# Kernel optimization log

Measured on AMD Instinct MI355X. Metric: run time of the kernel, lower is better.

The kernel has to match this reference:

```python
import jax, jax.numpy as jnp
import numpy as np
from jax import lax

ALPHA = 0.5
KERNEL = 25
NUM_P = 16
SEQ_LEN = 1440
PRED_LEN = 720
DWT_LEN = SEQ_LEN // 2 + 2            # 722 (pytorch_wavelets zero-mode, sym3 filt len 6)
FREQ = int(np.ceil(DWT_LEN / 2 * ALPHA) * 2)  # 362

_DEC_LO = np.array([0.035226291882100656, -0.08544127388224149, -0.13501102001039084,
                    0.4598775021193313, 0.8068915093133388, 0.3326705529509569], np.float32)
_DEC_HI = np.array([-0.3326705529509569, 0.8068915093133388, -0.4598775021193313,
                    -0.13501102001039084, 0.08544127388224149, 0.035226291882100656], np.float32)
DEC_LO, DEC_HI = jnp.asarray(_DEC_LO), jnp.asarray(_DEC_HI)
REC_LO, REC_HI = DEC_LO[::-1], DEC_HI[::-1]


def dwt1(x):
    # pytorch_wavelets DWT1DForward(J=1, mode='zero'): zero-pad then stride-2 true conv with dec filters
    B, C, L = x.shape
    out = (L + 5) // 2
    p = 2 * (out - 1) - L + 6
    xp = jnp.pad(x.reshape(B * C, 1, L), ((0, 0), (0, 0), (p // 2, p - p // 2)))
    ker = jnp.stack([DEC_LO[::-1], DEC_HI[::-1]])[:, None, :]   # (2,1,6); xcorr w/ reversed == conv
    y = lax.conv_general_dilated(xp, ker, (2,), 'VALID', dimension_numbers=('NCH', 'OIH', 'NCH'))
    return y[:, 0].reshape(B, C, out), y[:, 1].reshape(B, C, out)


def iwt1(lo, hi):
    # DWT1DInverse mode='zero': conv_transpose stride 2, padding L-2  ->  dilate + conv, pad 1
    B, C, n = lo.shape
    z = jnp.concatenate([lo.reshape(B * C, 1, n), hi.reshape(B * C, 1, n)], axis=1)
    ker = jnp.stack([REC_LO[::-1], REC_HI[::-1]])[None, :, :]   # (O=1, I=2, 6)
    y = lax.conv_general_dilated(z, ker, (1,), [(1, 1)], lhs_dilation=(2,),
                                 dimension_numbers=('NCH', 'OIH', 'NCH'))
    return y[:, 0].reshape(B, C, 2 * n - 4)


def mov_avg(x, k=KERNEL):
    pooled = lax.reduce_window(x, 0.0, lax.add, (1, 1, k), (1, 1, 1), 'VALID') / k
    return jnp.pad(pooled, ((0, 0), (0, 0), (k // 2, k // 2 - (k + 1) % 2)), mode='edge')


def mov_norm(x):
    mean = lax.stop_gradient(mov_avg(x))
    xc = lax.stop_gradient(x - mean)
    std = lax.stop_gradient(mov_avg(jnp.abs(xc))) + 1e-5
    return xc / std, mean, std


def inst_norm(x):
    mean = lax.stop_gradient(jnp.mean(x, -1, keepdims=True))
    xc = x - mean
    var = jnp.mean((xc - jnp.mean(xc, -1, keepdims=True)) ** 2, -1, keepdims=True)
    return xc / jnp.sqrt(var + 1e-5)


def mean_std_mlp(mean, std, mp, sp, mw1, mw2, sw1, sw2, mpred, spred):
    m_all = jnp.mean(mean, -1, keepdims=True)
    s_all = jnp.mean(std, -1, keepdims=True)
    mr = (mean - m_all) @ mp.T
    sr = (std - s_all) @ sp.T
    mr = jax.nn.relu(mr @ mw1.T) @ mw2.T
    sr = jax.nn.relu(sr @ sw1.T) @ sw2.T
    mean_o = mr @ mpred.T + m_all
    std_o = jax.nn.relu(sr @ spred.T + s_all) + 1e-5
    return mean_o, std_o


def forward(x, latent_w, latent_b, acp, dcp):
    xt = jnp.swapaxes(x, -1, 1)                    # (B, C, L)
    ac0, dc0 = dwt1(xt)                            # (B, C, DWT_LEN)
    ac_n = inst_norm(ac0)
    ac, m_ac, s_ac = mov_norm(ac0)
    dc, m_dc, s_dc = mov_norm(dc0)
    m_ac, s_ac = mean_std_mlp(m_ac, s_ac, *acp)    # MLPs[-1]
    m_dc, s_dc = mean_std_mlp(m_dc, s_dc, *dcp)    # MLPs[0]
    dcF = jnp.fft.fft(dc)
    acF = jnp.fft.fft(ac_n)
    idx = jnp.argsort(-jnp.abs(acF), axis=-1)[..., :FREQ]
    amp = ALPHA * jnp.take_along_axis(acF, idx, -1) + (1.0 - ALPHA) * jnp.take_along_axis(dcF, idx, -1)
    B, C, _ = dcF.shape
    bi = jnp.arange(B)[:, None, None]
    ci = jnp.arange(C)[None, :, None]
    dcF = dcF.at[bi, ci, idx].set(amp)
    dc = jnp.real(jnp.fft.ifft(dcF))
    xr = iwt1(ac, dc)                              # (B, C, SEQ_LEN)
    mean = iwt1(m_ac, m_dc)                        # (B, C, PRED_LEN)
    std = iwt1(s_ac, s_dc)
    xr = xr.reshape(B, C, NUM_P, SEQ_LEN // NUM_P)
    emb = xr @ latent_w.T + latent_b               # (B, C, NUM_P, d_model)
    return emb, mean, std


def setup_inputs() -> dict:
    key = jax.random.key(0)
    B, C = 64, 128
    d_model, d_ff = 512, 1024
    s = 0.02
    names_shapes = [
        ('x', (B, SEQ_LEN, C), 1.0),
        ('latent_w', (d_model, SEQ_LEN // NUM_P), s),
    ]
    for pre in ('ac', 'dc'):
        names_shapes += [
            (pre + '_mean_proj', (d_model, DWT_LEN), s),
            (pre + '_std_proj', (d_model, DWT_LEN), s),
            (pre + '_mean_ffn_w1', (d_ff, d_model), s),
            (pre + '_mean_ffn_w2', (d_model, d_ff), s),
            (pre + '_std_ffn_w1', (d_ff, d_model), s),
            (pre + '_std_ffn_w2', (d_model, d_ff), s),
            (pre + '_mean_pred', (PRED_LEN // 2 + 2, d_model), s),
            (pre + '_std_pred', (PRED_LEN // 2 + 2, d_model), s),
        ]
    keys = jax.random.split(key, len(names_shapes))
    inp = {n: jax.random.normal(k, shp, dtype=jnp.float32) * sc
           for (n, shp, sc), k in zip(names_shapes, keys)}
    inp['latent_b'] = jnp.zeros((d_model,), jnp.float32)
    return inp


def reference(x, latent_w, latent_b,
              ac_mean_proj, ac_std_proj, ac_mean_ffn_w1, ac_mean_ffn_w2,
              ac_std_ffn_w1, ac_std_ffn_w2, ac_mean_pred, ac_std_pred,
              dc_mean_proj, dc_std_proj, dc_mean_ffn_w1, dc_mean_ffn_w2,
              dc_std_ffn_w1, dc_std_ffn_w2, dc_mean_pred, dc_std_pred):
    acp = (ac_mean_proj, ac_std_proj, ac_mean_ffn_w1, ac_mean_ffn_w2,
           ac_std_ffn_w1, ac_std_ffn_w2, ac_mean_pred, ac_std_pred)
    dcp = (dc_mean_proj, dc_std_proj, dc_mean_ffn_w1, dc_mean_ffn_w2,
           dc_std_ffn_w1, dc_std_ffn_w2, dc_mean_pred, dc_std_pred)
    return forward(x, latent_w, latent_b, acp, dcp)
```

## Files before the change

### kernel.cpp

```cpp
#include <hip/hip_runtime.h>
#include <cmath>

#define RTOT 8192
#define NDWT 722
#define KP1  736
#define LSEQ 1440
#define NHEAD 362
#define NFREQ 362

typedef __bf16 bf16x8 __attribute__((ext_vector_type(8)));
typedef float f32x4 __attribute__((ext_vector_type(4)));
typedef float f32x2 __attribute__((ext_vector_type(2)));

__device__ __forceinline__ unsigned short f2bf(float f) {
    unsigned u = __float_as_uint(f);
    u += 0x7fffu + ((u >> 16) & 1u);
    return (unsigned short)(u >> 16);
}
__device__ __forceinline__ float bf2f(unsigned short u) {
    return __uint_as_float(((unsigned)u) << 16);
}

__device__ __forceinline__ void cmac(f32x2& s, f32x2 a, f32x2 w) {
    asm("v_pk_fma_f32 %0, %1, %2, %0 op_sel:[0,0,0] op_sel_hi:[0,1,1]\n\t"
        "v_pk_fma_f32 %0, %1, %2, %0 op_sel:[1,1,0] op_sel_hi:[1,0,1] neg_lo:[0,1,0]"
        : "+v"(s) : "v"(a), "v"(w));
}
__device__ __forceinline__ void cmac2(f32x2& s, f32x2 u, f32x2 v, f32x2 w) {
    asm("v_pk_fma_f32 %0, %1, %3, %0 op_sel:[0,0,0] op_sel_hi:[1,0,1]\n\t"
        "v_pk_fma_f32 %0, %2, %3, %0 op_sel:[1,1,0] op_sel_hi:[0,1,1] neg_lo:[0,1,0]"
        : "+v"(s) : "v"(u), "v"(v), "v"(w));
}
__device__ __forceinline__ f32x2 cmul(f32x2 a, f32x2 b) {
    f32x2 r;
    asm("v_pk_mul_f32 %0, %1, %2 op_sel:[0,0] op_sel_hi:[0,1]\n\t"
        "v_pk_fma_f32 %0, %1, %2, %0 op_sel:[1,1,0] op_sel_hi:[1,0,1] neg_lo:[0,1,0]"
        : "=&v"(r) : "v"(a), "v"(b));
    return r;
}

__constant__ float c_lo[6] = {0.035226291882100656f, -0.08544127388224149f, -0.13501102001039084f,
                              0.4598775021193313f, 0.8068915093133388f, 0.3326705529509569f};
__constant__ float c_hi[6] = {-0.3326705529509569f, 0.8068915093133388f, -0.4598775021193313f,
                              -0.13501102001039084f, 0.08544127388224149f, 0.035226291882100656f};

struct CvtDesc { const float* src; unsigned short* dst; int N, K, Np, Kp; };
struct CvtArgs { CvtDesc d[17]; float2* wtab; };
__global__ __launch_bounds__(256) void cvt_all_kernel(CvtArgs a) {
    if (blockIdx.y == 17) {
        int m = blockIdx.x * 256 + threadIdx.x;
        if (m < NDWT) {
            double ang = -2.0 * 3.141592653589793238462643383279502884 * (double)m / (double)NDWT;
            a.wtab[m] = make_float2((float)cos(ang), (float)sin(ang));
        }
        return;
    }
    CvtDesc d = a.d[blockIdx.y];
    int idx = blockIdx.x * 256 + threadIdx.x;
    int tot = d.Np * d.Kp;
    if (idx >= tot) return;
    int r = idx / d.Kp, c = idx - r * d.Kp;
    float v = (r < d.N && c < d.K) ? d.src[(size_t)r * d.K + c] : 0.f;
    d.dst[idx] = f2bf(v);
}

__global__ __launch_bounds__(256) void dwt_kernel(const float* __restrict__ x,
                                                  float* __restrict__ ac0,
                                                  float* __restrict__ dc0) {
    __shared__ float xs[68][129];
    const int b = blockIdx.x;
    const int t0 = blockIdx.y * 32;
    const int tid = threadIdx.x;
    const int lbase = 2 * t0 - 4;
    for (int i = tid; i < 68 * 32; i += 256) {
        int ri = i >> 5;
        int c4 = (i & 31) * 4;
        int l = lbase + ri;
        float4 v = make_float4(0.f, 0.f, 0.f, 0.f);
        if (l >= 0 && l < LSEQ)
            v = *reinterpret_cast<const float4*>(&x[((size_t)b * LSEQ + l) * 128 + c4]);
        xs[ri][c4] = v.x; xs[ri][c4 + 1] = v.y; xs[ri][c4 + 2] = v.z; xs[ri][c4 + 3] = v.w;
    }
    __syncthreads();
    const int tt = tid & 31;
    const int t = t0 + tt;
    const int cw = tid >> 5;
    if (t < NDWT) {
        #pragma unroll 4
        for (int co = 0; co < 16; co++) {
            int c = co * 8 + cw;
            float slo = 0.f, shi = 0.f;
            #pragma unroll
            for (int j = 0; j < 6; j++) {
                float v = xs[2 * tt + 5 - j][c];
                slo += v * c_lo[j];
                shi += v * c_hi[j];
            }
            size_t o = ((size_t)b * 128 + c) * NDWT + t;
            ac0[o] = slo;
            dc0[o] = shi;
        }
    }
}

__device__ __forceinline__ float blockSum256(float v, float* red) {
    #pragma unroll
    for (int o = 32; o > 0; o >>= 1) v += __shfl_down(v, o, 64);
    int lane = threadIdx.x & 63, wid = threadIdx.x >> 6;
    __syncthreads();
    if (lane == 0) red[wid] = v;
    __syncthreads();
    return red[0] + red[1] + red[2] + red[3];
}

template <bool ABS>
__device__ __forceinline__ void pool25(const float* rowv, float* pool, int tid) {
    int i0 = tid * 3;
    if (i0 < 698) {
        float s25 = 0.f;
        #pragma unroll
        for (int j = 0; j < 25; j++) { float v = rowv[i0 + j]; s25 += ABS ? fabsf(v) : v; }
        pool[i0] = s25 * (1.f / 25.f);
        #pragma unroll
        for (int qq = 1; qq < 3; qq++) {
            int i = i0 + qq;
            if (i < 698) {
                float vin = rowv[i + 24], vout = rowv[i - 1];
                s25 += (ABS ? fabsf(vin) : vin) - (ABS ? fabsf(vout) : vout);
                pool[i] = s25 * (1.f / 25.f);
            }
        }
    }
}

__device__ void fft722_dev(f32x2* X, f32x2* T, const f32x2* Wt, const f32x2* W19) {
    const int tid = threadIdx.x;
    if (tid < 190) {
        const int c = tid / 38;
        const int g = tid - c * 38;
        const int p = (g >= 19) ? 1 : 0;
        const int rr = g - 19 * p;
        const int t0 = c * 4;
        const int nt = (c == 4) ? 3 : 4;
        const f32x2* xp = X + 2 * rr + p;
        f32x2 st[4], w[4], s[4];
        f32x2 a0 = xp[0];
        #pragma unroll
        for (int i = 0; i < 4; i++) {
            int ti = t0 + i; if (ti > 18) ti = 0;
            st[i] = W19[ti];
            w[i] = st[i];
            s[i] = a0;
        }
        #pragma unroll
        for (int m = 1; m <= 9; m++) {
            f32x2 a = xp[38 * m];
            f32x2 b = xp[38 * (19 - m)];
            f32x2 u = a + b, v = a - b;
            #pragma unroll
            for (int i = 0; i < 4; i++) {
                cmac2(s[i], u, v, w[i]);
                if (m < 9) w[i] = cmul(w[i], st[i]);
            }
        }
        int m0 = rr * t0;
        f32x2* Tp = T + p * 361 + rr * 19 + t0;
        #pragma unroll
        for (int i = 0; i < 4; i++) {
            if (i < nt) Tp[i] = cmul(s[i], Wt[2 * m0]);
            m0 += rr;
        }
    }
    __syncthreads();
    if (tid < 190) {
        const int c = tid / 38;
        const int g = tid - c * 38;
        const int p = (g >= 19) ? 1 : 0;
        const int t = g - 19 * p;
        const int jj0 = c * 4;
        const int nj = (c == 4) ? 3 : 4;
        const f32x2* Ap = T + p * 361 + t;
        f32x2 st[4], w[4], s[4];
        f32x2 a0 = Ap[0];
        #pragma unroll
        for (int i = 0; i < 4; i++) {
            int jj = jj0 + i; if (jj > 18) jj = 0;
            st[i] = W19[jj];
            w[i] = st[i];
            s[i] = a0;
        }
        #pragma unroll
        for (int m = 1; m <= 9; m++) {
            f32x2 a = Ap[19 * m];
            f32x2 b = Ap[19 * (19 - m)];
            f32x2 u = a + b, v = a - b;
            #pragma unroll
            for (int i = 0; i < 4; i++) {
                cmac2(s[i], u, v, w[i]);
                if (m < 9) w[i] = cmul(w[i], st[i]);
            }
        }
        f32x2* Xp = X + p * 361;
        #pragma unroll
        for (int i = 0; i < 4; i++) {
            int jj = jj0 + i;
            if (i < nj) Xp[t + 19 * jj] = s[i];
        }
    }
    __syncthreads();
    for (int k = tid; k < 361; k += 256) {
        f32x2 e = X[k], o = X[361 + k], w = Wt[k];
        f32x2 tt = {0.f, 0.f};
        cmac(tt, o, w);
        X[k] = e + tt;
        X[361 + k] = e - tt;
    }
    __syncthreads();
}

__global__ __launch_bounds__(256) void stats_fft_kernel(
    const float* __restrict__ ac0in,
    const float* __restrict__ dc0in,
    unsigned short* __restrict__ cent,
    float* __restrict__ stat,
    unsigned short* __restrict__ xrbf,
    const f32x2* __restrict__ Wtab) {
    __shared__ f32x2 Wt[NDWT];
    __shared__ f32x2 W19s[19];
    __shared__ f32x2 B1[NDWT];
    __shared__ float acpL[NDWT];
    __shared__ __align__(16) char arena[8704];
    __shared__ unsigned hist[256];
    __shared__ unsigned suf[256];
    __shared__ unsigned sh_digit, sh_rem;
    f32x2* B2   = (f32x2*)arena;
    float* smag = (float*)(arena + 5776);
    float* row  = (float*)arena;
    float* xc   = (float*)(arena + 2888);
    float* pool = (float*)(arena + 5776);
    float* red  = (float*)(arena + 8568);
    const int r = blockIdx.x, tid = threadIdx.x;
    const int lane = tid & 63;
    const size_t base = (size_t)r * NDWT;
    const size_t baseP = (size_t)r * KP1;
    const size_t CS = (size_t)RTOT * KP1;

    for (int i = tid; i < NDWT; i += 256) Wt[i] = Wtab[i];
    if (tid < 19) W19s[tid] = Wtab[38 * tid];

    for (int i = tid; i < NDWT; i += 256) row[i] = ac0in[base + i];
    __syncthreads();
    float s = 0.f;
    for (int i = tid; i < NDWT; i += 256) s += row[i];
    float mean = blockSum256(s, red) * (1.f / 722.f);
    s = 0.f;
    for (int i = tid; i < NDWT; i += 256) s += row[i] - mean;
    float m2 = blockSum256(s, red) * (1.f / 722.f);
    s = 0.f;
    for (int i = tid; i < NDWT; i += 256) { float d = row[i] - mean - m2; s += d * d; }
    float var = blockSum256(s, red) * (1.f / 722.f);
    float inv = 1.f / sqrtf(var + 1e-5f);
    for (int i = tid; i < NDWT; i += 256) B1[i].x = (row[i] - mean) * inv;

    pool25<false>(row, pool, tid);
    __syncthreads();
    float msum = 0.f;
    for (int l = tid; l < NDWT; l += 256) {
        int pi = l - 12; pi = pi < 0 ? 0 : (pi > 697 ? 697 : pi);
        float m = pool[pi];
        msum += m;
        xc[l] = row[l] - m;
    }
    float m_all = blockSum256(msum, red) * (1.f / 722.f);
    __syncthreads();
    pool25<true>(xc, pool, tid);
    __syncthreads();
    float ssum = 0.f;
    for (int l = tid; l < NDWT; l += 256) {
        int pi = l - 12; pi = pi < 0 ? 0 : (pi > 697 ? 697 : pi);
        float sd = pool[pi] + 1e-5f;
        ssum += sd;
        acpL[l] = xc[l] / sd;
    }
    float s_all = blockSum256(ssum, red) * (1.f / 722.f);
    if (tid == 0) { stat[r] = m_all; stat[RTOT + r] = s_all; }
    for (int l = tid; l < KP1; l += 256) {
        if (l < NDWT) {
            float m = row[l] - xc[l];
            int pi = l - 12; pi = pi < 0 ? 0 : (pi > 697 ? 697 : pi);
            float sd = pool[pi] + 1e-5f;
            cent[baseP + l]      = f2bf(m - m_all);
            cent[CS + baseP + l] = f2bf(sd - s_all);
        } else { cent[baseP + l] = 0; cent[CS + baseP + l] = 0; }
    }
    __syncthreads();

    for (int i = tid; i < NDWT; i += 256) row[i] = dc0in[base + i];
    __syncthreads();
    pool25<false>(row, pool, tid);
    __syncthreads();
    float msum2 = 0.f;
    for (int l = tid; l < NDWT; l += 256) {
        int pi = l - 12; pi = pi < 0 ? 0 : (pi > 697 ? 697 : pi);
        float m = pool[pi];
        msum2 += m;
        xc[l] = row[l] - m;
    }
    float m_all2 = blockSum256(msum2, red) * (1.f / 722.f);
    __syncthreads();
    pool25<true>(xc, pool, tid);
    __syncthreads();
    float ssum2 = 0.f;
    for (int l = tid; l < NDWT; l += 256) {
        int pi = l - 12; pi = pi < 0 ? 0 : (pi > 697 ? 697 : pi);
        float sd = pool[pi] + 1e-5f;
        ssum2 += sd;
        B1[l].y = xc[l] / sd;
    }
    float s_all2 = blockSum256(ssum2, red) * (1.f / 722.f);
    if (tid == 0) { stat[2 * RTOT + r] = m_all2; stat[3 * RTOT + r] = s_all2; }
    for (int l = tid; l < KP1; l += 256) {
        if (l < NDWT) {
            float m = row[l] - xc[l];
            int pi = l - 12; pi = pi < 0 ? 0 : (pi > 697 ? 697 : pi);
            float sd = pool[pi] + 1e-5f;
            cent[2 * CS + baseP + l] = f2bf(m - m_all2);
            cent[3 * CS + baseP + l] = f2bf(sd - s_all2);
        } else { cent[2 * CS + baseP + l] = 0; cent[3 * CS + baseP + l] = 0; }
    }
    __syncthreads();

    fft722_dev(B1, B2, Wt, W19s);
    for (int k = tid; k < 362; k += 256) {
        int m = (NDWT - k) % NDWT;
        f32x2 zk = B1[k], zm = B1[m];
        f32x2 ak = {0.5f * (zk.x + zm.x), 0.5f * (zk.y - zm.y)};
        f32x2 dk = {0.5f * (zk.y + zm.y), 0.5f * (zm.x - zk.x)};
        B1[k] = ak; B2[k] = dk;
        smag[k] = ak.x * ak.x + ak.y * ak.y;
        if (m != k) {
            f32x2 am = {0.5f * (zm.x + zk.x), 0.5f * (zm.y - zk.y)};
            f32x2 dm = {0.5f * (zm.y + zk.y), 0.5f * (zk.x - zm.x)};
            B1[m] = am; B2[m] = dm;
            smag[m] = am.x * am.x + am.y * am.y;
        }
    }
    __syncthreads();

    unsigned prefix = 0, rem = NFREQ;
    for (int shift = 24; shift >= 0; shift -= 8) {
        hist[tid] = 0;
        __syncthreads();
        unsigned hm = (shift == 24) ? 0u : (0xFFFFFFFFu << (shift + 8));
        for (int i = tid; i < NDWT; i += 256) {
            unsigned b = __float_as_uint(smag[i]);
            if ((b & hm) == prefix) atomicAdd(&hist[(b >> shift) & 255], 1u);
        }
        __syncthreads();
        if (tid < 64) {
            unsigned h0 = hist[tid * 4 + 0], h1 = hist[tid * 4 + 1];
            unsigned h2 = hist[tid * 4 + 2], h3 = hist[tid * 4 + 3];
            unsigned tot = h0 + h1 + h2 + h3;
            unsigned tinc = tot;
            #pragma unroll
            for (int off = 1; off < 64; off <<= 1) {
                unsigned v = __shfl_down(tinc, off, 64);
                tinc += (lane + off < 64) ? v : 0u;
            }
            unsigned tail = tinc - tot;
            unsigned S3 = tail + h3;
            unsigned S2 = S3 + h2;
            unsigned S1 = S2 + h1;
            unsigned S0 = S1 + h0;
            if (S0 >= rem && S1 < rem) { sh_digit = (unsigned)(tid * 4 + 0); sh_rem = rem - S1; }
            if (S1 >= rem && S2 < rem) { sh_digit = (unsigned)(tid * 4 + 1); sh_rem = rem - S2; }
            if (S2 >= rem && S3 < rem) { sh_digit = (unsigned)(tid * 4 + 2); sh_rem = rem - S3; }
            if (S3 >= rem && tail < rem) { sh_digit = (unsigned)(tid * 4 + 3); sh_rem = rem - tail; }
        }
        __syncthreads();
        prefix |= (sh_digit << shift);
        rem = sh_rem;
    }
    int c0 = tid * 3, cnt = 0;
    #pragma unroll
    for (int j = 0; j < 3; j++) {
        int i = c0 + j;
        if (i < NDWT && __float_as_uint(smag[i]) == prefix) cnt++;
    }
    suf[tid] = (unsigned)cnt;
    __syncthreads();
    if (tid < 64) {
        unsigned p0 = suf[tid * 4 + 0], p1 = suf[tid * 4 + 1];
        unsigned p2 = suf[tid * 4 + 2], p3 = suf[tid * 4 + 3];
        unsigned tot = p0 + p1 + p2 + p3;
        unsigned pinc = tot;
        #pragma unroll
        for (int off = 1; off < 64; off <<= 1) {
            unsigned v = __shfl_up(pinc, off, 64);
            pinc += (lane >= off) ? v : 0u;
        }
        unsigned head = pinc - tot;
        suf[tid * 4 + 0] = head;
        suf[tid * 4 + 1] = head + p0;
        suf[tid * 4 + 2] = head + p0 + p1;
        suf[tid * 4 + 3] = head + p0 + p1 + p2;
    }
    __syncthreads();
    int myexc = (int)suf[tid], o = 0;
    #pragma unroll
    for (int j = 0; j < 3; j++) {
        int i = c0 + j;
        if (i < NDWT) {
            unsigned b = __float_as_uint(smag[i]);
            int f = (b > prefix) ? 1 : 0;
            if (b == prefix) { if ((unsigned)(myexc + o) < rem) f = 1; o++; }
            smag[i] = f ? 1.f : 0.f;
        }
    }
    __syncthreads();

    for (int i = tid; i < NDWT; i += 256) {
        f32x2 d = B2[i];
        if (smag[i] != 0.f) { f32x2 a = B1[i]; d.x = 0.5f * (a.x + d.x); d.y = 0.5f * (a.y + d.y); }
        B1[i] = f32x2{d.x, -d.y};
    }
    __syncthreads();
    fft722_dev(B1, B2, Wt, W19s);

    const float inv722 = 1.f / 722.f;
    if (tid < 96) {
        int sub = tid / 6, c = 90 + tid % 6;
        xrbf[((size_t)r * 16 + sub) * 96 + c] = 0;
    }
    for (int t = tid; t < LSEQ; t += 256) {
        float sx = 0.f;
        if (t & 1) {
            int j0 = (t - 1) >> 1;
            #pragma unroll
            for (int i = 0; i < 3; i++)
                sx += acpL[j0 + i] * c_lo[2 * i] + (B1[j0 + i].x * inv722) * c_hi[2 * i];
        } else {
            int j0 = t >> 1;
            #pragma unroll
            for (int i = 0; i < 3; i++)
                sx += acpL[j0 + i] * c_lo[2 * i + 1] + (B1[j0 + i].x * inv722) * c_hi[2 * i + 1];
        }
        xrbf[((size_t)r * 16 + t / 90) * 96 + (t % 90)] = f2bf(sx);
    }
}

__global__ __launch_bounds__(256) void iwt_heads_kernel(const unsigned short* __restrict__ heads,
                                                        float* __restrict__ out_mean,
                                                        float* __restrict__ out_std) {
    const int r = blockIdx.x;
    const int y = blockIdx.y;
    const int z = y / 3;
    const int t = (y % 3) * 256 + threadIdx.x;
    if (t >= 720) return;
    const size_t HR = (size_t)RTOT * NHEAD;
    const unsigned short* lp = heads + (size_t)z * HR + (size_t)r * NHEAD;
    const unsigned short* hp = heads + (size_t)(2 + z) * HR + (size_t)r * NHEAD;
    float* out = (z ? out_std : out_mean) + (size_t)r * 720;
    float s = 0.f;
    if (t & 1) {
        int j0 = (t - 1) >> 1;
        #pragma unroll
        for (int i = 0; i < 3; i++) s += bf2f(lp[j0 + i]) * c_lo[2 * i] + bf2f(hp[j0 + i]) * c_hi[2 * i];
    } else {
        int j0 = t >> 1;
        #pragma unroll
        for (int i = 0; i < 3; i++) s += bf2f(lp[j0 + i]) * c_lo[2 * i + 1] + bf2f(hp[j0 + i]) * c_hi[2 * i + 1];
    }
    out[t] = s;
}

struct ZPtrs { const unsigned short* p[4]; };
template <int EPI>
__global__ __launch_bounds__(256) void mfma_gemm_z(
    const unsigned short* __restrict__ A, int lda, size_t zsA,
    ZPtrs Wz, int ldw,
    void* __restrict__ Cout, int ldc, size_t zsC, int Nc,
    const float* __restrict__ biasBase, const float* __restrict__ cbias,
    int Ksteps) {
    __shared__ unsigned short As[2][128 * 32];
    __shared__ unsigned short Bs[2][128 * 32];
    const int z = blockIdx.z;
    const unsigned short* Az = A + (size_t)z * zsA;
    const unsigned short* W = Wz.p[z];
    const int tid = threadIdx.x;
    const int lane = tid & 63, wid = tid >> 6;
    const int bm = blockIdx.x * 128, bn = blockIdx.y * 128;
    const int wr = (wid >> 1) * 64, wc = (wid & 1) * 64;
    f32x4 acc[4][4] = {};
    const int srow = (lane >> 2);
    const int scol = (lane & 3) * 8;
    const int ch0 = wid * 2, ch1 = wid * 2 + 1;
    const unsigned short* ga0 = Az + (size_t)(bm + ch0 * 16 + srow) * lda + scol;
    const unsigned short* ga1 = Az + (size_t)(bm + ch1 * 16 + srow) * lda + scol;
    const unsigned short* gb0 = W + (size_t)(bn + ch0 * 16 + srow) * ldw + scol;
    const unsigned short* gb1 = W + (size_t)(bn + ch1 * 16 + srow) * ldw + scol;

#define STAGE_GL(buf, ks) do { const int k0_ = (ks) * 32;                                      \
    __builtin_amdgcn_global_load_lds((const __attribute__((address_space(1))) unsigned int*)(ga0 + k0_), \
        (__attribute__((address_space(3))) unsigned int*)(&As[buf][ch0 * 512]), 16, 0, 0);     \
    __builtin_amdgcn_global_load_lds((const __attribute__((address_space(1))) unsigned int*)(gb0 + k0_), \
        (__attribute__((address_space(3))) unsigned int*)(&Bs[buf][ch0 * 512]), 16, 0, 0);     \
    __builtin_amdgcn_global_load_lds((const __attribute__((address_space(1))) unsigned int*)(ga1 + k0_), \
        (__attribute__((address_space(3))) unsigned int*)(&As[buf][ch1 * 512]), 16, 0, 0);     \
    __builtin_amdgcn_global_load_lds((const __attribute__((address_space(1))) unsigned int*)(gb1 + k0_), \
        (__attribute__((address_space(3))) unsigned int*)(&Bs[buf][ch1 * 512]), 16, 0, 0);     \
    } while (0)

    STAGE_GL(0, 0);
    int cur = 0;
    const int kof = (lane >> 4) * 8;
    for (int ks = 0; ks < Ksteps; ks++) {
        if (ks + 1 < Ksteps) {
            STAGE_GL(cur ^ 1, ks + 1);
            asm volatile("s_waitcnt vmcnt(4)" ::: "memory");
        } else {
            asm volatile("s_waitcnt vmcnt(0)" ::: "memory");
        }
        __builtin_amdgcn_s_barrier();
        __builtin_amdgcn_sched_barrier(0);
        bf16x8 af[4], bfr[4];
        #pragma unroll
        for (int m = 0; m < 4; m++)
            af[m] = *reinterpret_cast<const bf16x8*>(&As[cur][(wr + m * 16 + (lane & 15)) * 32 + kof]);
        #pragma unroll
        for (int n = 0; n < 4; n++)
            bfr[n] = *reinterpret_cast<const bf16x8*>(&Bs[cur][(wc + n * 16 + (lane & 15)) * 32 + kof]);
        #pragma unroll
        for (int m = 0; m < 4; m++)
            #pragma unroll
            for (int n = 0; n < 4; n++)
                acc[m][n] = __builtin_amdgcn_mfma_f32_16x16x32_bf16(af[m], bfr[n], acc[m][n], 0, 0, 0);
        __builtin_amdgcn_s_barrier();
        __builtin_amdgcn_sched_barrier(0);
        cur ^= 1;
    }
#undef STAGE_GL

    unsigned short* Cb = (unsigned short*)Cout + (size_t)z * zsC;
    float* Cf = (float*)Cout + (size_t)z * zsC;
    const int crow0 = bm + wr + (lane >> 4) * 4;
    const int ccol0 = bn + wc + (lane & 15);
    #pragma unroll
    for (int m = 0; m < 4; m++) {
        #pragma unroll
        for (int n = 0; n < 4; n++) {
            const int col = ccol0 + n * 16;
            if (col < Nc) {
                #pragma unroll
                for (int q = 0; q < 4; q++) {
                    const int row = crow0 + m * 16 + q;
                    float v = acc[m][n][q];
                    if (EPI == 0) {
                        Cb[(size_t)row * ldc + col] = f2bf(v);
                    } else if (EPI == 1) {
                        Cb[(size_t)row * ldc + col] = f2bf(fmaxf(v, 0.f));
                    } else if (EPI == 4) {
                        Cf[(size_t)row * ldc + col] = v + cbias[col];
                    } else {
                        float ob = biasBase[(size_t)z * RTOT + row];
                        if (z & 1) v = fmaxf(v + ob, 0.f) + 1e-5f;
                        else       v += ob;
                        Cb[(size_t)row * ldc + col] = f2bf(v);
                    }
                }
            }
        }
    }
}

extern "C" void kernel_launch(void* const* d_in, const int* in_sizes, int n_in,
                              void* d_out, int out_size, void* d_ws, size_t ws_size,
                              hipStream_t stream) {
    const float* x = (const float*)d_in[0];
    const float* latent_w = (const float*)d_in[1];
    int p0;
    const float* latent_b;
    if (n_in > 2 && in_sizes[2] == 512) { latent_b = (const float*)d_in[2]; p0 = 3; }
    else                                { latent_b = (const float*)d_in[18]; p0 = 2; }

    char* wp = (char*)d_ws;
    auto alloc = [&](size_t bytes) { char* p = wp; wp += (bytes + 255) & ~(size_t)255; return p; };
    const size_t RN = (size_t)RTOT * NDWT;
    float* ac0b = (float*)alloc(RN * 4);
    float* dc0b = (float*)alloc(RN * 4);
    float* stat = (float*)alloc(4 * RTOT * 4);
    float2* Wtab = (float2*)alloc(NDWT * 8);
    unsigned short* cent  = (unsigned short*)alloc((size_t)4 * RTOT * KP1 * 2);
    unsigned short* xrbf  = (unsigned short*)alloc((size_t)131072 * 96 * 2);
    unsigned short* mlpB4 = (unsigned short*)alloc((size_t)4 * RTOT * 512 * 2);
    unsigned short* mlpA4 = (unsigned short*)alloc((size_t)4 * RTOT * 1024 * 2);
    unsigned short* mlpC4 = (unsigned short*)alloc((size_t)4 * RTOT * 512 * 2);
    unsigned short* heads = mlpB4;
    unsigned short *projW[4], *w1W[4], *w2W[4], *predW[4];
    for (int z = 0; z < 4; z++) {
        projW[z] = (unsigned short*)alloc((size_t)512 * KP1 * 2);
        w1W[z]   = (unsigned short*)alloc((size_t)1024 * 512 * 2);
        w2W[z]   = (unsigned short*)alloc((size_t)512 * 1024 * 2);
        predW[z] = (unsigned short*)alloc((size_t)384 * 512 * 2);
    }
    unsigned short* latwb = (unsigned short*)alloc((size_t)512 * 96 * 2);
    (void)ws_size;

    CvtArgs ca;
    int si = 0;
    for (int z = 0; z < 4; z++) {
        int branch = z >> 1, isStd = z & 1, wb = p0 + branch * 8;
        ca.d[si++] = {(const float*)d_in[wb + isStd],         projW[z], 512, NDWT, 512, KP1};
        ca.d[si++] = {(const float*)d_in[wb + 2 + 2 * isStd], w1W[z], 1024, 512, 1024, 512};
        ca.d[si++] = {(const float*)d_in[wb + 3 + 2 * isStd], w2W[z], 512, 1024, 512, 1024};
        ca.d[si++] = {(const float*)d_in[wb + 6 + isStd],     predW[z], NHEAD, 512, 384, 512};
    }
    ca.d[16] = {latent_w, latwb, 512, 90, 512, 96};
    ca.wtab = Wtab;
    cvt_all_kernel<<<dim3(2048, 18), dim3(256), 0, stream>>>(ca);

    dwt_kernel<<<dim3(64, 23), dim3(256), 0, stream>>>(x, ac0b, dc0b);
    stats_fft_kernel<<<dim3(RTOT), dim3(256), 0, stream>>>(
        ac0b, dc0b, cent, stat, xrbf, (const f32x2*)Wtab);

    float* out = (float*)d_out;
    ZPtrs Zl = {{latwb, latwb, latwb, latwb}};
    mfma_gemm_z<4><<<dim3(1024, 4, 1), dim3(256), 0, stream>>>(
        xrbf, 96, 0, Zl, 96, out, 512, 0, 512, nullptr, latent_b, 3);

    ZPtrs Zp = {{projW[0], projW[1], projW[2], projW[3]}};
    ZPtrs Z1 = {{w1W[0], w1W[1], w1W[2], w1W[3]}};
    ZPtrs Z2 = {{w2W[0], w2W[1], w2W[2], w2W[3]}};
    ZPtrs Zh = {{predW[0], predW[1], predW[2], predW[3]}};
    mfma_gemm_z<0><<<dim3(64, 4, 4), dim3(256), 0, stream>>>(
        cent, KP1, (size_t)RTOT * KP1, Zp, KP1, mlpB4, 512, (size_t)RTOT * 512, 512, nullptr, nullptr, KP1 / 32);
    mfma_gemm_z<1><<<dim3(64, 8, 4), dim3(256), 0, stream>>>(
        mlpB4, 512, (size_t)RTOT * 512, Z1, 512, mlpA4, 1024, (size_t)RTOT * 1024, 1024, nullptr, nullptr, 16);
    mfma_gemm_z<0><<<dim3(64, 4, 4), dim3(256), 0, stream>>>(
        mlpA4, 1024, (size_t)RTOT * 1024, Z2, 1024, mlpC4, 512, (size_t)RTOT * 512, 512, nullptr, nullptr, 32);
    mfma_gemm_z<5><<<dim3(64, 3, 4), dim3(256), 0, stream>>>(
        mlpC4, 512, (size_t)RTOT * 512, Zh, 512, heads, NHEAD, (size_t)RTOT * NHEAD, NHEAD, stat, nullptr, 16);

    float* out_mean = out + (size_t)67108864;
    float* out_std  = out_mean + (size_t)5898240;
    iwt_heads_kernel<<<dim3(RTOT, 6), dim3(256), 0, stream>>>(heads, out_mean, out_std);
}
```

Before: 509.0 us.

## Replace inverse 722-point FFT with half-length complex FFT for real output

The inverse transform only needs the real part, so the spectrum is made Hermitian-symmetric and folded into a 361-point complex sequence. Even and odd outputs come back as the real and imaginary parts of a 361-point FFT. This roughly halves the inverse FFT work in the stats kernel. It adds a folding pass with twiddle multiplies and changes the mask mixing to a symmetric average, which could slightly alter results if the mask is not symmetric.

```diff
diff --git a/kernel.cpp b/kernel.cpp
--- a/kernel.cpp
+++ b/kernel.cpp
@@ -214,6 +214,78 @@
         cmac(tt, o, w);
         X[k] = e + tt;
         X[361 + k] = e - tt;
+    }
+    __syncthreads();
+}
+
+__device__ void fft361_dev(f32x2* X, f32x2* T, const f32x2* Wt, const f32x2* W19) {
+    const int tid = threadIdx.x;
+    if (tid < 95) {
+        const int a = tid / 5;
+        const int ch = tid % 5;
+        const int t0 = ch * 4;
+        const int nt = (ch == 4) ? 3 : 4;
+        const f32x2* xp = X + a;
+        f32x2 st[4], w[4], s[4];
+        f32x2 a0 = xp[0];
+        #pragma unroll
+        for (int i = 0; i < 4; i++) {
+            int ti = t0 + i; if (ti > 18) ti = 0;
+            st[i] = W19[ti];
+            w[i] = st[i];
+            s[i] = a0;
+        }
+        #pragma unroll
+        for (int m = 1; m <= 9; m++) {
+            f32x2 aa = xp[19 * m];
+            f32x2 bb = xp[19 * (19 - m)];
+            f32x2 u = aa + bb, v = aa - bb;
+            #pragma unroll
+            for (int i = 0; i < 4; i++) {
+                cmac2(s[i], u, v, w[i]);
+                if (m < 9) w[i] = cmul(w[i], st[i]);
+            }
+        }
+        int m0 = a * t0;
+        f32x2* Tp = T + a * 19 + t0;
+        #pragma unroll
+        for (int i = 0; i < 4; i++) {
+            if (i < nt) Tp[i] = cmul(s[i], Wt[2 * m0]);
+            m0 += a;
+        }
+    }
+    __syncthreads();
+    if (tid < 95) {
+        const int t = tid / 5;
+        const int ch = tid % 5;
+        const int c0 = ch * 4;
+        const int nc = (ch == 4) ? 3 : 4;
+        const f32x2* Ap = T + t;
+        f32x2 st[4], w[4], s[4];
+        f32x2 a0 = Ap[0];
+        #pragma unroll
+        for (int i = 0; i < 4; i++) {
+            int cc = c0 + i; if (cc > 18) cc = 0;
+            st[i] = W19[cc];
+            w[i] = st[i];
+            s[i] = a0;
+        }
+        #pragma unroll
+        for (int m = 1; m <= 9; m++) {
+            f32x2 aa = Ap[19 * m];
+            f32x2 bb = Ap[19 * (19 - m)];
+            f32x2 u = aa + bb, v = aa - bb;
+            #pragma unroll
+            for (int i = 0; i < 4; i++) {
+                cmac2(s[i], u, v, w[i]);
+                if (m < 9) w[i] = cmul(w[i], st[i]);
+            }
+        }
+        #pragma unroll
+        for (int i = 0; i < 4; i++) {
+            int cc = c0 + i;
+            if (i < nc) X[t + 19 * cc] = s[i];
+        }
     }
     __syncthreads();
 }
@@ -419,13 +491,24 @@
     }
     __syncthreads();
 
-    for (int i = tid; i < NDWT; i += 256) {
-        f32x2 d = B2[i];
-        if (smag[i] != 0.f) { f32x2 a = B1[i]; d.x = 0.5f * (a.x + d.x); d.y = 0.5f * (a.y + d.y); }
-        B1[i] = f32x2{d.x, -d.y};
-    }
-    __syncthreads();
-    fft722_dev(B1, B2, Wt, W19s);
+    for (int k = tid; k < 361; k += 256) {
+        int k2 = k + 361;
+        int p1i = (NDWT - k) % NDWT;
+        int p2i = NDWT - k2;
+        float w1 = 0.5f * (smag[k] + smag[p1i]);
+        float w2 = 0.5f * (smag[k2] + smag[p2i]);
+        f32x2 a1 = B1[k], d1 = B2[k];
+        f32x2 a2 = B1[k2], d2 = B2[k2];
+        f32x2 m1 = { d1.x + w1 * 0.5f * (a1.x - d1.x), d1.y + w1 * 0.5f * (a1.y - d1.y) };
+        f32x2 mB = { d2.x + w2 * 0.5f * (a2.x - d2.x), d2.y + w2 * 0.5f * (a2.y - d2.y) };
+        f32x2 E = m1 + mB;
+        f32x2 D = m1 - mB;
+        f32x2 wc = Wt[k];
+        f32x2 O = { D.x * wc.x + D.y * wc.y, D.y * wc.x - D.x * wc.y };
+        B1[k] = f32x2{ E.x - O.y, -(E.y + O.x) };
+    }
+    __syncthreads();
+    fft361_dev(B1, B2, Wt, W19s);
 
     const float inv722 = 1.f / 722.f;
     if (tid < 96) {
@@ -437,13 +520,21 @@
         if (t & 1) {
             int j0 = (t - 1) >> 1;
             #pragma unroll
-            for (int i = 0; i < 3; i++)
-                sx += acpL[j0 + i] * c_lo[2 * i] + (B1[j0 + i].x * inv722) * c_hi[2 * i];
+            for (int i = 0; i < 3; i++) {
+                int j = j0 + i;
+                f32x2 z = B1[j >> 1];
+                float dm = ((j & 1) ? -z.y : z.x) * inv722;
+                sx += acpL[j] * c_lo[2 * i] + dm * c_hi[2 * i];
+            }
         } else {
             int j0 = t >> 1;
             #pragma unroll
-            for (int i = 0; i < 3; i++)
-                sx += acpL[j0 + i] * c_lo[2 * i + 1] + (B1[j0 + i].x * inv722) * c_hi[2 * i + 1];
+            for (int i = 0; i < 3; i++) {
+                int j = j0 + i;
+                f32x2 z = B1[j >> 1];
+                float dm = ((j & 1) ? -z.y : z.x) * inv722;
+                sx += acpL[j] * c_lo[2 * i + 1] + dm * c_hi[2 * i + 1];
+            }
         }
         xrbf[((size_t)r * 16 + t / 90) * 96 + (t % 90)] = f2bf(sx);
     }
```

Result: no change. 507.9 us (-0.2%).
